# Optimization experiments

Hardware: AMD Instinct MI355X
Metric: run time of the kernel (lower is better)

Reference implementation:

```python
import jax, jax.numpy as jnp
import numpy as np

B, S, D, H, DK = 2, 2048, 256, 8, 32


def setup_inputs() -> dict:
    key = jax.random.key(0)
    ks = jax.random.split(key, 12)
    inp = {
        "query": jax.random.normal(ks[0], (B, S, D), jnp.float32),
        "key_": jax.random.normal(ks[1], (B, S, D), jnp.float32),
        "value": jax.random.normal(ks[2], (B, S, D), jnp.float32),
        "mask": jax.random.randint(ks[3], (B, S, S), 0, 2).astype(bool),
        "relation": jax.random.normal(ks[4], (B, S, S), jnp.float32) * 0.05,
        # learned params (Linear stores y = x @ W^T; we store W already transposed)
        "Wq": jax.random.normal(ks[5], (D, H * DK), jnp.float32) * 0.02,
        "Wk": jax.random.normal(ks[6], (D, H * DK), jnp.float32) * 0.02,
        "Wv": jax.random.normal(ks[7], (D, H * DK), jnp.float32) * 0.02,
        "Wfc": jax.random.normal(ks[8], (H * DK, D), jnp.float32) * 0.02,
        "bfc": jax.random.normal(ks[9], (D,), jnp.float32) * 0.02,
        "gamma": jnp.ones((D,), jnp.float32),
        "beta": jnp.zeros((D,), jnp.float32),
    }
    return inp


def _layernorm(x, gamma, beta, eps=1e-5):
    mu = jnp.mean(x, axis=-1, keepdims=True)
    var = jnp.var(x, axis=-1, keepdims=True)
    return (x - mu) * jax.lax.rsqrt(var + eps) * gamma + beta


def reference(query, key_, value, mask, relation, Wq, Wk, Wv, Wfc, bfc, gamma, beta):
    b, s, _ = query.shape
    def split_heads(x, W):
        return (x @ W).reshape(b, s, H, DK).transpose(0, 2, 1, 3)  # [B,H,S,DK]
    Q = split_heads(query, Wq)
    K = split_heads(key_, Wk)
    V = split_heads(value, Wv)
    # (Q K^T) @ relation / sqrt(dk)   -- relation broadcast over heads
    qk = jnp.einsum('bhqd,bhkd->bhqk', Q, K)          # [B,H,S,S]
    scores = jnp.einsum('bhqk,bkn->bhqn', qk, relation) / jnp.sqrt(jnp.float32(DK))
    scores = jnp.where(mask[:, None, :, :], jnp.float32(-1e9), scores)
    attn = jax.nn.softmax(scores, axis=-1)            # dropout in eval mode = identity
    att = jnp.einsum('bhqn,bhnd->bhqd', attn, V)      # [B,H,S,DK]
    att = att.transpose(0, 2, 1, 3).reshape(b, s, H * DK)
    out = att @ Wfc + bfc
    return _layernorm(out + query, gamma, beta), attn
```

## Files before the change

### kernel.cpp

```cpp
#include <hip/hip_runtime.h>

constexpr int Bc = 2, Sc = 2048, Dc = 256, Hc = 8, DKc = 32;
constexpr int BH = Bc * Hc;

typedef _Float16 f16x8 __attribute__((ext_vector_type(8)));
typedef _Float16 f16x4 __attribute__((ext_vector_type(4)));
typedef float    f32x4 __attribute__((ext_vector_type(4)));

__global__ __launch_bounds__(256) void proj3_kernel(
    const float* __restrict__ query, const float* __restrict__ key_,
    const float* __restrict__ value, const float* __restrict__ Wq,
    const float* __restrict__ Wk, const float* __restrict__ Wv,
    _Float16* __restrict__ Qb, _Float16* __restrict__ Kt,
    _Float16* __restrict__ Vt)
{
    constexpr int ROWS = 8;
    __shared__ float xs[ROWS][Dc];
    const int z = blockIdx.y;
    const float* X = (z == 0) ? query : (z == 1) ? key_ : value;
    const float* W = (z == 0) ? Wq : (z == 1) ? Wk : Wv;
    _Float16* out = (z == 0) ? Qb : (z == 1) ? Kt : Vt;
    const int vtrans = (z != 0);
    const float scale = (z == 0) ? 0.17677669529663689f : 1.0f;

    const int r0 = blockIdx.x * ROWS;
    const int t = threadIdx.x;
    #pragma unroll
    for (int i = 0; i < ROWS; ++i)
        xs[i][t] = X[(long)(r0 + i) * Dc + t];
    __syncthreads();
    float acc[ROWS];
    #pragma unroll
    for (int i = 0; i < ROWS; ++i) acc[i] = 0.f;
    for (int d = 0; d < Dc; ++d) {
        float w = W[d * Dc + t];
        #pragma unroll
        for (int i = 0; i < ROWS; ++i) acc[i] = fmaf(xs[i][d], w, acc[i]);
    }
    const int h = t >> 5, dk = t & 31;
    #pragma unroll
    for (int i = 0; i < ROWS; ++i) {
        int row = r0 + i;
        int b = row / Sc, s = row % Sc;
        long idx = vtrans ? (((long)(b * Hc + h) * DKc + dk) * Sc + s)
                          : (((long)(b * Hc + h) * Sc + s) * DKc + dk);
        out[idx] = (_Float16)(acc[i] * scale);
    }
}

__global__ __launch_bounds__(256) void relT_kernel(
    const float* __restrict__ rel, _Float16* __restrict__ relT)
{
    __shared__ float tile[64][65];
    const int b = blockIdx.z;
    const int k0 = blockIdx.y * 64, n0 = blockIdx.x * 64;
    const int tx = threadIdx.x & 63, ty = threadIdx.x >> 6;
    const float* src = rel + (long)b * Sc * Sc;
    #pragma unroll
    for (int i = 0; i < 16; ++i) {
        int k = i * 4 + ty;
        tile[k][tx] = src[(long)(k0 + k) * Sc + n0 + tx];
    }
    __syncthreads();
    _Float16* dst = relT + (long)b * Sc * Sc;
    #pragma unroll
    for (int i = 0; i < 16; ++i) {
        int n = i * 4 + ty;
        dst[(long)(n0 + n) * Sc + k0 + tx] = (_Float16)tile[tx][n];
    }
}

__global__ __launch_bounds__(256) void maskpack_kernel(
    const unsigned int* __restrict__ m, unsigned int* __restrict__ out)
{
    const int idx = blockIdx.x * 256 + threadIdx.x;
    const uint4 a = ((const uint4*)m)[idx * 2];
    const uint4 b = ((const uint4*)m)[idx * 2 + 1];
    unsigned int ws[8] = {a.x, a.y, a.z, a.w, b.x, b.y, b.z, b.w};
    unsigned int r = 0;
    #pragma unroll
    for (int j = 0; j < 8; ++j) {
        unsigned int nib = (ws[j] | (ws[j] >> 7) | (ws[j] >> 14) | (ws[j] >> 21)) & 0xFu;
        r |= nib << (4 * j);
    }
    out[idx] = r;
}

__global__ __launch_bounds__(256) void kr_kernel(
    const _Float16* __restrict__ relT, const _Float16* __restrict__ Kt,
    _Float16* __restrict__ KRT)
{
    constexpr int LDK = 72;
    __shared__ _Float16 As[64][LDK];
    __shared__ _Float16 Bs[64][LDK];
    const int b = blockIdx.z;
    const int m0 = blockIdx.y * 64;
    const int n0 = blockIdx.x * 64;
    const _Float16* Ap = relT + (long)b * Sc * Sc;
    const _Float16* Bp = Kt + (long)b * Hc * DKc * Sc;
    const int t = threadIdx.x;
    const int lane = t & 63, wave = t >> 6;
    const int wr = wave >> 1, wc = wave & 1;
    const int c = lane & 15, g = lane >> 4;
    const int lrow = t >> 2;
    const int lcol = (t & 3) * 16;
    f32x4 acc[2][2] = {};
    for (int k0 = 0; k0 < Sc; k0 += 64) {
        *(f16x8*)&As[lrow][lcol]     = *(const f16x8*)&Ap[(long)(m0 + lrow) * Sc + k0 + lcol];
        *(f16x8*)&As[lrow][lcol + 8] = *(const f16x8*)&Ap[(long)(m0 + lrow) * Sc + k0 + lcol + 8];
        *(f16x8*)&Bs[lrow][lcol]     = *(const f16x8*)&Bp[(long)(n0 + lrow) * Sc + k0 + lcol];
        *(f16x8*)&Bs[lrow][lcol + 8] = *(const f16x8*)&Bp[(long)(n0 + lrow) * Sc + k0 + lcol + 8];
        __syncthreads();
        #pragma unroll
        for (int kk = 0; kk < 2; ++kk) {
            const int kb = kk * 32 + g * 8;
            f16x8 af[2], bf[2];
            #pragma unroll
            for (int m = 0; m < 2; ++m)
                af[m] = *(const f16x8*)&As[wr * 32 + m * 16 + c][kb];
            #pragma unroll
            for (int n = 0; n < 2; ++n)
                bf[n] = *(const f16x8*)&Bs[wc * 32 + n * 16 + c][kb];
            #pragma unroll
            for (int m = 0; m < 2; ++m)
                #pragma unroll
                for (int n = 0; n < 2; ++n)
                    acc[m][n] = __builtin_amdgcn_mfma_f32_16x16x32_f16(
                        af[m], bf[n], acc[m][n], 0, 0, 0);
        }
        __syncthreads();
    }
    _Float16* outp = KRT + (long)b * Sc * 256;
    #pragma unroll
    for (int m = 0; m < 2; ++m)
        #pragma unroll
        for (int n = 0; n < 2; ++n)
            #pragma unroll
            for (int i = 0; i < 4; ++i) {
                int row = m0 + wr * 32 + m * 16 + g * 4 + i;
                int col = n0 + wc * 32 + n * 16 + c;
                outp[(long)row * 256 + col] = (_Float16)acc[m][n][i];
            }
}

__global__ __launch_bounds__(256) void attn_pv_kernel(
    const _Float16* __restrict__ Qb,
    const _Float16* __restrict__ KRT,
    const _Float16* __restrict__ Vt,
    const unsigned int* __restrict__ mbits,
    float* __restrict__ rinvg,
    float* __restrict__ attw)
{
    constexpr int NT = 128, LDP = 136;
    __shared__ _Float16 p_lds[64][LDP];
    const int bh = blockIdx.y;
    const int b = bh >> 3, h = bh & 7;
    const int q0 = blockIdx.x * 64;
    const int t = threadIdx.x, lane = t & 63, w = t >> 6;
    const int c = lane & 15, g = lane >> 4;
    const int q = q0 + w * 16 + c;
    const f16x8 qf = *(const f16x8*)&Qb[((long)bh * Sc + q) * DKc + g * 8];
    const _Float16* krt = KRT + (long)b * Sc * 256 + h * 32;
    const unsigned int* mbitrow = mbits + ((long)b * Sc + q) * (Sc / 32);
    const f32x4 zero = {};
    f32x4 acc[2] = {};
    float esum = 0.f;

    for (int nt = 0; nt < Sc / NT; ++nt) {
        const int n0 = nt * NT;
        f32x4 s[8];
        #pragma unroll
        for (int nf = 0; nf < 8; ++nf) {
            f16x8 kf = *(const f16x8*)&krt[(long)(n0 + nf * 16 + c) * 256 + g * 8];
            s[nf] = __builtin_amdgcn_mfma_f32_16x16x32_f16(kf, qf, zero, 0, 0, 0);
        }
        const uint4 mq = *(const uint4*)&mbitrow[nt * 4];
        const unsigned int mwv[4] = {mq.x, mq.y, mq.z, mq.w};
        #pragma unroll
        for (int nf = 0; nf < 8; ++nf) {
            const unsigned int bits = mwv[nf >> 1] >> ((nf & 1) * 16 + g * 4);
            f16x4 pv;
            #pragma unroll
            for (int i = 0; i < 4; ++i) {
                float p = ((bits >> i) & 1u) ? 0.f : __expf(s[nf][i]);
                esum += p;
                pv[i] = (_Float16)p;
            }
            *(f16x4*)&p_lds[w * 16 + c][nf * 16 + g * 4] = pv;
        }
        #pragma unroll
        for (int ks = 0; ks < 4; ++ks) {
            f16x8 af = *(const f16x8*)&p_lds[w * 16 + c][ks * 32 + g * 8];
            #pragma unroll
            for (int nb = 0; nb < 2; ++nb) {
                f16x8 vf = *(const f16x8*)&Vt[((long)bh * DKc + nb * 16 + c) * Sc + n0 + ks * 32 + g * 8];
                acc[nb] = __builtin_amdgcn_mfma_f32_16x16x32_f16(af, vf, acc[nb], 0, 0, 0);
            }
        }
    }
    esum += __shfl_xor(esum, 16);
    esum += __shfl_xor(esum, 32);
    const float rinv = 1.f / esum;
    if (lane < 16)
        rinvg[(long)bh * Sc + q0 + w * 16 + lane] = rinv;
    #pragma unroll
    for (int nb = 0; nb < 2; ++nb)
        #pragma unroll
        for (int i = 0; i < 4; ++i) {
            const float rs = __shfl(rinv, g * 4 + i);
            attw[((long)(b * Sc + q0 + w * 16 + g * 4 + i)) * Dc + h * 32 + nb * 16 + c]
                = acc[nb][i] * rs;
        }
}

__global__ __launch_bounds__(256) void attn_store_kernel(
    const _Float16* __restrict__ Qb,
    const _Float16* __restrict__ KRT,
    const unsigned int* __restrict__ mbits,
    const float* __restrict__ rinvg,
    float* __restrict__ attn_out)
{
    constexpr int LDA = 132;
    __shared__ float a_lds[4][16][LDA];
    const int nt = blockIdx.x;
    const int q0 = blockIdx.y * 64;
    const int bh = blockIdx.z;
    const int b = bh >> 3, h = bh & 7;
    const int t = threadIdx.x, lane = t & 63, w = t >> 6;
    const int c = lane & 15, g = lane >> 4;
    const int q = q0 + w * 16 + c;
    const int n0 = nt * 128;
    const f16x8 qf = *(const f16x8*)&Qb[((long)bh * Sc + q) * DKc + g * 8];
    const _Float16* krt = KRT + (long)b * Sc * 256 + h * 32;
    const float rinv = rinvg[(long)bh * Sc + q];
    const f32x4 zero = {};

    f32x4 s[8];
    #pragma unroll
    for (int nf = 0; nf < 8; ++nf) {
        f16x8 kf = *(const f16x8*)&krt[(long)(n0 + nf * 16 + c) * 256 + g * 8];
        s[nf] = __builtin_amdgcn_mfma_f32_16x16x32_f16(kf, qf, zero, 0, 0, 0);
    }
    const uint4 mq = *(const uint4*)&mbits[((long)b * Sc + q) * (Sc / 32) + nt * 4];
    const unsigned int mwv[4] = {mq.x, mq.y, mq.z, mq.w};
    #pragma unroll
    for (int nf = 0; nf < 8; ++nf) {
        const unsigned int bits = mwv[nf >> 1] >> ((nf & 1) * 16 + g * 4);
        f32x4 av;
        #pragma unroll
        for (int i = 0; i < 4; ++i)
            av[i] = ((bits >> i) & 1u) ? 0.f : __expf(s[nf][i]) * rinv;
        *(f32x4*)&a_lds[w][c][nf * 16 + g * 4] = av;
    }
    float* aoutw = attn_out + (long)bh * Sc * Sc
                 + (long)(q0 + w * 16 + (lane >> 5)) * Sc + (lane & 31) * 4 + n0;
    #pragma unroll
    for (int r2 = 0; r2 < 8; ++r2) {
        f32x4 v = *(const f32x4*)&a_lds[w][r2 * 2 + (lane >> 5)][(lane & 31) * 4];
        __builtin_nontemporal_store(v, (f32x4*)&aoutw[(long)(r2 * 2) * Sc]);
    }
}

__global__ __launch_bounds__(256) void out_kernel(
    const float* __restrict__ att, const float* __restrict__ Wfc,
    const float* __restrict__ bfc, const float* __restrict__ query,
    const float* __restrict__ gamma, const float* __restrict__ beta,
    float* __restrict__ out)
{
    __shared__ float xs[4][Dc];
    __shared__ float ys[4][Dc];
    const int r0 = blockIdx.x * 4;
    const int t = threadIdx.x;
    #pragma unroll
    for (int i = 0; i < 4; ++i) xs[i][t] = att[(long)(r0 + i) * Dc + t];
    __syncthreads();
    float acc[4] = {0.f, 0.f, 0.f, 0.f};
    for (int d = 0; d < Dc; ++d) {
        float wv = Wfc[d * Dc + t];
        #pragma unroll
        for (int i = 0; i < 4; ++i) acc[i] = fmaf(xs[i][d], wv, acc[i]);
    }
    const float bias = bfc[t];
    #pragma unroll
    for (int i = 0; i < 4; ++i)
        ys[i][t] = acc[i] + bias + query[(long)(r0 + i) * Dc + t];
    __syncthreads();
    const int w = t >> 6, lane = t & 63;
    float x0 = ys[w][lane], x1 = ys[w][lane + 64];
    float x2 = ys[w][lane + 128], x3 = ys[w][lane + 192];
    float sum = x0 + x1 + x2 + x3;
    float sq = x0 * x0 + x1 * x1 + x2 * x2 + x3 * x3;
    for (int off = 32; off; off >>= 1) {
        sum += __shfl_down(sum, off);
        sq  += __shfl_down(sq, off);
    }
    sum = __shfl(sum, 0);
    sq  = __shfl(sq, 0);
    const float mu = sum * (1.f / 256.f);
    const float var = sq * (1.f / 256.f) - mu * mu;
    const float rstd = rsqrtf(var + 1e-5f);
    float* orow = out + (long)(r0 + w) * Dc;
    orow[lane]       = (x0 - mu) * rstd * gamma[lane]       + beta[lane];
    orow[lane + 64]  = (x1 - mu) * rstd * gamma[lane + 64]  + beta[lane + 64];
    orow[lane + 128] = (x2 - mu) * rstd * gamma[lane + 128] + beta[lane + 128];
    orow[lane + 192] = (x3 - mu) * rstd * gamma[lane + 192] + beta[lane + 192];
}

extern "C" void kernel_launch(void* const* d_in, const int* in_sizes, int n_in,
                              void* d_out, int out_size, void* d_ws, size_t ws_size,
                              hipStream_t stream)
{
    const float* query   = (const float*)d_in[0];
    const float* key_    = (const float*)d_in[1];
    const float* value   = (const float*)d_in[2];
    const unsigned int* mask = (const unsigned int*)d_in[3];
    const float* relation = (const float*)d_in[4];
    const float* Wq  = (const float*)d_in[5];
    const float* Wk  = (const float*)d_in[6];
    const float* Wv  = (const float*)d_in[7];
    const float* Wfc = (const float*)d_in[8];
    const float* bfc = (const float*)d_in[9];
    const float* gamma = (const float*)d_in[10];
    const float* beta  = (const float*)d_in[11];

    float* out_ln   = (float*)d_out;
    float* out_attn = (float*)d_out + (size_t)Bc * Sc * Dc;

    char* ws = (char*)d_ws;
    _Float16* Qb   = (_Float16*)(ws + 0);
    _Float16* Kt   = (_Float16*)(ws + 2097152);
    _Float16* Vt   = (_Float16*)(ws + 4194304);
    _Float16* relT = (_Float16*)(ws + 6291456);
    _Float16* KRT  = (_Float16*)(ws + 23068672);
    float*    attw = (float*)   (ws + 25165824);
    unsigned int* mbits = (unsigned int*)(ws + 29360128);
    float*    rinvg = (float*)  (ws + 30408704);

    proj3_kernel<<<dim3(Bc * Sc / 8, 3), 256, 0, stream>>>(
        query, key_, value, Wq, Wk, Wv, Qb, Kt, Vt);
    relT_kernel<<<dim3(Sc / 64, Sc / 64, Bc), 256, 0, stream>>>(relation, relT);
    maskpack_kernel<<<dim3(Bc * Sc * Sc / 32 / 256), 256, 0, stream>>>(mask, mbits);
    kr_kernel<<<dim3(4, Sc / 64, Bc), 256, 0, stream>>>(relT, Kt, KRT);
    attn_pv_kernel<<<dim3(Sc / 64, BH), 256, 0, stream>>>(
        Qb, KRT, Vt, mbits, rinvg, attw);
    attn_store_kernel<<<dim3(Sc / 128, Sc / 64, BH), 256, 0, stream>>>(
        Qb, KRT, mbits, rinvg, out_attn);
    out_kernel<<<dim3(Bc * Sc / 4), 256, 0, stream>>>(attw, Wfc, bfc, query,
                                                      gamma, beta, out_ln);
}
```

Before: 208.0 us.

## Split-K the KR GEMM and attention PV kernels, vectorize relation transpose

The KR GEMM and the attention PV pass each split their reduction dimension into two halves. This doubles the grid so more of the GPU's compute units stay busy. Each half writes fp32 partial results, and two small new combine kernels add the halves, then cast to fp16 or normalise by the summed softmax denominators. The relation transpose kernel also switches to 4-wide vector loads and stores. The trade-off is extra launches and extra global traffic for the partial buffers.

```diff
diff --git a/kernel.cpp b/kernel.cpp
--- a/kernel.cpp
+++ b/kernel.cpp
@@ -54,19 +54,24 @@
     __shared__ float tile[64][65];
     const int b = blockIdx.z;
     const int k0 = blockIdx.y * 64, n0 = blockIdx.x * 64;
-    const int tx = threadIdx.x & 63, ty = threadIdx.x >> 6;
+    const int t = threadIdx.x;
+    const int r = t >> 4;
+    const int c4 = (t & 15) * 4;
     const float* src = rel + (long)b * Sc * Sc;
     #pragma unroll
-    for (int i = 0; i < 16; ++i) {
-        int k = i * 4 + ty;
-        tile[k][tx] = src[(long)(k0 + k) * Sc + n0 + tx];
+    for (int i = 0; i < 4; ++i) {
+        f32x4 v = *(const f32x4*)&src[(long)(k0 + i * 16 + r) * Sc + n0 + c4];
+        *(f32x4*)&tile[i * 16 + r][c4] = v;
     }
     __syncthreads();
     _Float16* dst = relT + (long)b * Sc * Sc;
     #pragma unroll
-    for (int i = 0; i < 16; ++i) {
-        int n = i * 4 + ty;
-        dst[(long)(n0 + n) * Sc + k0 + tx] = (_Float16)tile[tx][n];
+    for (int i = 0; i < 4; ++i) {
+        const int n = i * 16 + r;
+        f16x4 o;
+        #pragma unroll
+        for (int e = 0; e < 4; ++e) o[e] = (_Float16)tile[c4 + e][n];
+        *(f16x4*)&dst[(long)(n0 + n) * Sc + k0 + c4] = o;
     }
 }
 
@@ -88,12 +93,13 @@
 
 __global__ __launch_bounds__(256) void kr_kernel(
     const _Float16* __restrict__ relT, const _Float16* __restrict__ Kt,
-    _Float16* __restrict__ KRT)
+    float* __restrict__ KRp)
 {
     constexpr int LDK = 72;
     __shared__ _Float16 As[64][LDK];
     __shared__ _Float16 Bs[64][LDK];
-    const int b = blockIdx.z;
+    const int z = blockIdx.z;
+    const int b = z >> 1, ks = z & 1;
     const int m0 = blockIdx.y * 64;
     const int n0 = blockIdx.x * 64;
     const _Float16* Ap = relT + (long)b * Sc * Sc;
@@ -105,7 +111,7 @@
     const int lrow = t >> 2;
     const int lcol = (t & 3) * 16;
     f32x4 acc[2][2] = {};
-    for (int k0 = 0; k0 < Sc; k0 += 64) {
+    for (int k0 = ks * 1024; k0 < ks * 1024 + 1024; k0 += 64) {
         *(f16x8*)&As[lrow][lcol]     = *(const f16x8*)&Ap[(long)(m0 + lrow) * Sc + k0 + lcol];
         *(f16x8*)&As[lrow][lcol + 8] = *(const f16x8*)&Ap[(long)(m0 + lrow) * Sc + k0 + lcol + 8];
         *(f16x8*)&Bs[lrow][lcol]     = *(const f16x8*)&Bp[(long)(n0 + lrow) * Sc + k0 + lcol];
@@ -130,7 +136,7 @@
         }
         __syncthreads();
     }
-    _Float16* outp = KRT + (long)b * Sc * 256;
+    float* outp = KRp + ((long)ks * Bc + b) * Sc * 256;
     #pragma unroll
     for (int m = 0; m < 2; ++m)
         #pragma unroll
@@ -139,8 +145,21 @@
             for (int i = 0; i < 4; ++i) {
                 int row = m0 + wr * 32 + m * 16 + g * 4 + i;
                 int col = n0 + wc * 32 + n * 16 + c;
-                outp[(long)row * 256 + col] = (_Float16)acc[m][n][i];
+                outp[(long)row * 256 + col] = acc[m][n][i];
             }
+}
+
+__global__ __launch_bounds__(256) void krc_kernel(
+    const float* __restrict__ KRp, _Float16* __restrict__ KRT)
+{
+    const long idx = ((long)blockIdx.x * 256 + threadIdx.x) * 4;
+    const long half = (long)Bc * Sc * 256;
+    f32x4 a = *(const f32x4*)&KRp[idx];
+    f32x4 b = *(const f32x4*)&KRp[half + idx];
+    f16x4 o;
+    #pragma unroll
+    for (int i = 0; i < 4; ++i) o[i] = (_Float16)(a[i] + b[i]);
+    *(f16x4*)&KRT[idx] = o;
 }
 
 __global__ __launch_bounds__(256) void attn_pv_kernel(
@@ -148,12 +167,13 @@
     const _Float16* __restrict__ KRT,
     const _Float16* __restrict__ Vt,
     const unsigned int* __restrict__ mbits,
-    float* __restrict__ rinvg,
-    float* __restrict__ attw)
+    float* __restrict__ esum_p,
+    float* __restrict__ accp)
 {
     constexpr int NT = 128, LDP = 136;
     __shared__ _Float16 p_lds[64][LDP];
     const int bh = blockIdx.y;
+    const int ns = blockIdx.z;
     const int b = bh >> 3, h = bh & 7;
     const int q0 = blockIdx.x * 64;
     const int t = threadIdx.x, lane = t & 63, w = t >> 6;
@@ -166,7 +186,7 @@
     f32x4 acc[2] = {};
     float esum = 0.f;
 
-    for (int nt = 0; nt < Sc / NT; ++nt) {
+    for (int nt = ns * (1024 / NT); nt < (ns + 1) * (1024 / NT); ++nt) {
         const int n0 = nt * NT;
         f32x4 s[8];
         #pragma unroll
@@ -200,17 +220,34 @@
     }
     esum += __shfl_xor(esum, 16);
     esum += __shfl_xor(esum, 32);
-    const float rinv = 1.f / esum;
     if (lane < 16)
-        rinvg[(long)bh * Sc + q0 + w * 16 + lane] = rinv;
+        esum_p[((long)ns * BH + bh) * Sc + q0 + w * 16 + lane] = esum;
     #pragma unroll
     for (int nb = 0; nb < 2; ++nb)
         #pragma unroll
         for (int i = 0; i < 4; ++i) {
-            const float rs = __shfl(rinv, g * 4 + i);
-            attw[((long)(b * Sc + q0 + w * 16 + g * 4 + i)) * Dc + h * 32 + nb * 16 + c]
-                = acc[nb][i] * rs;
-        }
+            const long qrow = q0 + w * 16 + g * 4 + i;
+            accp[(((long)ns * BH + bh) * Sc + qrow) * 32 + nb * 16 + c] = acc[nb][i];
+        }
+}
+
+__global__ __launch_bounds__(256) void pvc_kernel(
+    const float* __restrict__ esum_p,
+    const float* __restrict__ accp,
+    float* __restrict__ attw,
+    float* __restrict__ rinvg)
+{
+    const int t = threadIdx.x;
+    const int qi = t >> 5, hd = t & 31;
+    const long row = (long)blockIdx.x * 8 + qi;
+    const int bh = (int)(row >> 11);
+    const int q = (int)(row & (Sc - 1));
+    const int b = bh >> 3, h = bh & 7;
+    const long half = (long)BH * Sc;
+    const float rinv = 1.f / (esum_p[row] + esum_p[half + row]);
+    const float a = accp[row * 32 + hd] + accp[half * 32 + row * 32 + hd];
+    attw[((long)(b * Sc + q)) * Dc + h * 32 + hd] = a * rinv;
+    if (hd == 0) rinvg[row] = rinv;
 }
 
 __global__ __launch_bounds__(256) void attn_store_kernel(
@@ -335,14 +372,19 @@
     float*    attw = (float*)   (ws + 25165824);
     unsigned int* mbits = (unsigned int*)(ws + 29360128);
     float*    rinvg = (float*)  (ws + 30408704);
+    float*    KRp   = (float*)  (ws + 30539776);
+    float*    esum_p= (float*)  (ws + 38928384);
+    float*    accp  = (float*)  (ws + 39190528);
 
     proj3_kernel<<<dim3(Bc * Sc / 8, 3), 256, 0, stream>>>(
         query, key_, value, Wq, Wk, Wv, Qb, Kt, Vt);
     relT_kernel<<<dim3(Sc / 64, Sc / 64, Bc), 256, 0, stream>>>(relation, relT);
     maskpack_kernel<<<dim3(Bc * Sc * Sc / 32 / 256), 256, 0, stream>>>(mask, mbits);
-    kr_kernel<<<dim3(4, Sc / 64, Bc), 256, 0, stream>>>(relT, Kt, KRT);
-    attn_pv_kernel<<<dim3(Sc / 64, BH), 256, 0, stream>>>(
-        Qb, KRT, Vt, mbits, rinvg, attw);
+    kr_kernel<<<dim3(4, Sc / 64, Bc * 2), 256, 0, stream>>>(relT, Kt, KRp);
+    krc_kernel<<<dim3(Bc * Sc * 256 / 4 / 256), 256, 0, stream>>>(KRp, KRT);
+    attn_pv_kernel<<<dim3(Sc / 64, BH, 2), 256, 0, stream>>>(
+        Qb, KRT, Vt, mbits, esum_p, accp);
+    pvc_kernel<<<dim3(BH * Sc / 8), 256, 0, stream>>>(esum_p, accp, attw, rinvg);
     attn_store_kernel<<<dim3(Sc / 128, Sc / 64, BH), 256, 0, stream>>>(
         Qb, KRT, mbits, rinvg, out_attn);
     out_kernel<<<dim3(Bc * Sc / 4), 256, 0, stream>>>(attw, Wfc, bfc, query,
```

Result: no change. 206.8 us (-0.6%).
